# Performance work log

Hardware: AMD Instinct MI355X
Metric: run time of the kernel (lower is better)

## Reference

```python
import jax, jax.numpy as jnp
import numpy as np

S, B, D, H = 2048, 2, 1024, 16
DK = D // H


def rotate_half(x):
    # interleaved variant: pairs (x0,x1)->(-x1,x0)
    x1 = x[..., ::2]
    x2 = x[..., 1::2]
    return jnp.stack((-x2, x1), axis=-1).reshape(x.shape)


def apply_rope(x):
    # x: [B, H, S, dk]
    b, h, s, dk = x.shape
    pos = jnp.arange(s, dtype=jnp.float32)
    inv_freq = 1.0 / (10000.0 ** (jnp.arange(0, dk, 2, dtype=jnp.float32) / dk))
    freqs = jnp.einsum('i,j->ij', pos, inv_freq)          # [S, dk/2]
    emb = jnp.concatenate((freqs, freqs), axis=-1)        # [S, dk]  (non-interleaved cos/sin, as in source)
    cos = jnp.cos(emb)[None, None, :, :]
    sin = jnp.sin(emb)[None, None, :, :]
    return x * cos + rotate_half(x) * sin


def setup_inputs() -> dict:
    key = jax.random.key(0)
    ks = jax.random.split(key, 11)
    sc = 0.02
    return {
        'query': jax.random.normal(ks[0], (S, B, D), jnp.float32),
        'key':   jax.random.normal(ks[1], (S, B, D), jnp.float32),
        'value': jax.random.normal(ks[2], (S, B, D), jnp.float32),
        'wq': jax.random.normal(ks[3], (D, D), jnp.float32) * sc,
        'bq': jax.random.normal(ks[4], (D,), jnp.float32) * sc,
        'wk': jax.random.normal(ks[5], (D, D), jnp.float32) * sc,
        'bk': jax.random.normal(ks[6], (D,), jnp.float32) * sc,
        'wv': jax.random.normal(ks[7], (D, D), jnp.float32) * sc,
        'bv': jax.random.normal(ks[8], (D,), jnp.float32) * sc,
        'wo': jax.random.normal(ks[9], (D, D), jnp.float32) * sc,
        'bo': jax.random.normal(ks[10], (D,), jnp.float32) * sc,
    }


def reference(query, key, value, wq, bq, wk, bk, wv, bv, wo, bo):
    s_q, b, _ = query.shape
    s_k = key.shape[0]

    def split_heads(x, s):
        # [S,B,D] -> [B,H,S,dk]
        return x.transpose(1, 0, 2).reshape(b, s, H, DK).transpose(0, 2, 1, 3)

    Q = split_heads(query @ wq.T + bq, s_q)
    K = split_heads(key @ wk.T + bk, s_k)
    V = split_heads(value @ wv.T + bv, s_k)

    Q = apply_rope(Q)
    K = apply_rope(K)

    scores = jnp.einsum('bhqd,bhkd->bhqk', Q, K) / jnp.sqrt(jnp.float32(DK))
    attn = jax.nn.softmax(scores, axis=-1)
    out = jnp.einsum('bhqk,bhkd->bhqd', attn, V)          # [B,H,Sq,dk]
    out = out.transpose(0, 2, 1, 3).reshape(b, s_q, D)    # [B,Sq,D]
    out = out.transpose(1, 0, 2)                          # [Sq,B,D]
    return out @ wo.T + bo
```

## Files before the change

### kernel.cpp

```cpp
#include <hip/hip_runtime.h>
#include <cstdint>
#include <cstddef>

typedef __attribute__((ext_vector_type(4))) float f32x4;
typedef __attribute__((ext_vector_type(8))) float f32x8;
typedef __attribute__((ext_vector_type(16))) float f32x16;
typedef __attribute__((ext_vector_type(8))) __bf16 bf16x8;
typedef __attribute__((ext_vector_type(4))) __bf16 bf16x4;
typedef __attribute__((ext_vector_type(2))) __bf16 bf16x2;
typedef __attribute__((ext_vector_type(4))) unsigned int u32x4;
typedef unsigned short u16;

#define S_LEN 2048
#define BATCH 2
#define DMODEL 1024
#define NHEAD 16
#define HDK 64

__device__ __forceinline__ u16 f2bf(float f) {
    uint32_t u = __float_as_uint(f);
    u += 0x7FFFu + ((u >> 16) & 1u);
    return (u16)(u >> 16);
}

__device__ __forceinline__ void gload_lds16(const void* g, void* l) {
    __builtin_amdgcn_global_load_lds(
        (const __attribute__((address_space(1))) uint32_t*)g,
        (__attribute__((address_space(3))) uint32_t*)l, 16, 0, 0);
}

__device__ __forceinline__ unsigned pk2(float a, float b) {
    bf16x2 t;
    t[0] = (__bf16)a; t[1] = (__bf16)b;
    return __builtin_bit_cast(unsigned, t);
}

__device__ __forceinline__ f32x16 z16() {
    f32x16 v = {0.f,0.f,0.f,0.f,0.f,0.f,0.f,0.f,0.f,0.f,0.f,0.f,0.f,0.f,0.f,0.f};
    return v;
}

__global__ __launch_bounds__(256) void cvt_kernel(
    const float* __restrict__ a0, const float* __restrict__ a1, const float* __restrict__ a2,
    const float* __restrict__ a3, const float* __restrict__ a4, const float* __restrict__ a5,
    const float* __restrict__ a6,
    u16* __restrict__ o0, u16* __restrict__ o1, u16* __restrict__ o2,
    u16* __restrict__ o3, u16* __restrict__ o4, u16* __restrict__ o5,
    u16* __restrict__ o6)
{
    const int by = blockIdx.y;
    const float* s;
    u16* d;
    int n;
    switch (by) {
        case 0: s = a0; d = o0; n = 4194304; break;
        case 1: s = a1; d = o1; n = 4194304; break;
        case 2: s = a2; d = o2; n = 4194304; break;
        case 3: s = a3; d = o3; n = 1048576; break;
        case 4: s = a4; d = o4; n = 1048576; break;
        case 5: s = a5; d = o5; n = 1048576; break;
        default: s = a6; d = o6; n = 1048576; break;
    }
    int idx = (blockIdx.x * 256 + threadIdx.x) * 8;
    if (idx >= n) return;
    float4 f0 = *(const float4*)(s + idx);
    float4 f1 = *(const float4*)(s + idx + 4);
    alignas(16) u16 o[8] = {f2bf(f0.x), f2bf(f0.y), f2bf(f0.z), f2bf(f0.w),
                            f2bf(f1.x), f2bf(f1.y), f2bf(f1.z), f2bf(f1.w)};
    *(u32x4*)(d + idx) = *(const u32x4*)o;
}

__global__ __launch_bounds__(512) void qkv_kernel(
    const u16* __restrict__ X0, const u16* __restrict__ X1, const u16* __restrict__ X2,
    const u16* __restrict__ W0, const u16* __restrict__ W1, const u16* __restrict__ W2,
    const float* __restrict__ B0, const float* __restrict__ B1, const float* __restrict__ B2,
    u16* __restrict__ O0, u16* __restrict__ O1, u16* __restrict__ O2)
{
    __shared__ __align__(16) u16 lA[2][128 * 64];
    __shared__ __align__(16) u16 lB[2][128 * 64];
    const int tid = threadIdx.x, wid = tid >> 6, lane = tid & 63;
    const int l15 = lane & 15, l4 = lane >> 4;
    const int p = blockIdx.y * 32 + blockIdx.x;
    const int vid = (p & 7) * 96 + (p >> 3);
    const int bx = vid & 31, byv = vid >> 5;
    const int mat = byv >> 3;
    const u16* X = mat == 0 ? X0 : (mat == 1 ? X1 : X2);
    const u16* W = mat == 0 ? W0 : (mat == 1 ? W1 : W2);
    const float* bias = mat == 0 ? B0 : (mat == 1 ? B1 : B2);
    u16* O = mat == 0 ? O0 : (mat == 1 ? O1 : O2);
    const int m0 = bx * 128, n0 = (byv & 7) * 128;
    const int mw = (wid >> 1) * 32, nw = (wid & 1) * 64;

    f32x4 acc[2][4];
#pragma unroll
    for (int i = 0; i < 2; ++i)
#pragma unroll
        for (int j = 0; j < 4; ++j) acc[i][j] = (f32x4){0.f, 0.f, 0.f, 0.f};

#define QSTAGE(bufi, k0_) do {                                                \
        _Pragma("unroll")                                                     \
        for (int it = 0; it < 2; ++it) {                                      \
            int cc = it * 512 + tid;                                          \
            int row = cc >> 3, g = (cc & 7) ^ (row & 7);                      \
            gload_lds16(X + (size_t)(m0 + row) * 1024 + (k0_) + g * 8,        \
                        (char*)lA + (bufi) * 16384 + (cc & ~63) * 16);        \
            gload_lds16(W + (size_t)(n0 + row) * 1024 + (k0_) + g * 8,        \
                        (char*)lB + (bufi) * 16384 + (cc & ~63) * 16);        \
        }                                                                     \
    } while (0)

    QSTAGE(0, 0);
    for (int ks = 0; ks < 16; ++ks) {
        const int cur = ks & 1;
        if (ks < 15) {
            QSTAGE(cur ^ 1, (ks + 1) * 64);
            asm volatile("s_waitcnt vmcnt(4)" ::: "memory");
        } else {
            asm volatile("s_waitcnt vmcnt(0)" ::: "memory");
        }
        __builtin_amdgcn_s_barrier();
        const char* la = (const char*)lA + cur * 16384;
        const char* lb = (const char*)lB + cur * 16384;
        __builtin_amdgcn_s_setprio(1);
#pragma unroll
        for (int kk = 0; kk < 2; ++kk) {
            bf16x8 af[2], bfr[4];
#pragma unroll
            for (int f = 0; f < 2; ++f) {
                int ra = mw + f * 16 + l15;
                af[f] = *(const bf16x8*)(la + ra * 128 +
                        ((kk * 64 + l4 * 16) ^ ((ra & 7) << 4)));
            }
#pragma unroll
            for (int f = 0; f < 4; ++f) {
                int rb = nw + f * 16 + l15;
                bfr[f] = *(const bf16x8*)(lb + rb * 128 +
                        ((kk * 64 + l4 * 16) ^ ((rb & 7) << 4)));
            }
#pragma unroll
            for (int mf = 0; mf < 2; ++mf)
#pragma unroll
                for (int nf = 0; nf < 4; ++nf)
                    acc[mf][nf] = __builtin_amdgcn_mfma_f32_16x16x32_bf16(
                        af[mf], bfr[nf], acc[mf][nf], 0, 0, 0);
        }
        __builtin_amdgcn_s_setprio(0);
        __builtin_amdgcn_s_barrier();
    }
#undef QSTAGE

#pragma unroll
    for (int mf = 0; mf < 2; ++mf) {
#pragma unroll
        for (int nf = 0; nf < 4; ++nf) {
            int gcol = n0 + nw + nf * 16 + l15;
            float bval = bias[gcol];
            int h = gcol >> 6, d = gcol & 63;
            float invf = __expf(-(float)(d & 31) * 0.2878231366f);
#pragma unroll
            for (int i = 0; i < 4; ++i) {
                int grow = m0 + mw + mf * 16 + l4 * 4 + i;
                int s = grow >> 1, b = grow & 1;
                float v = acc[mf][nf][i] + bval;
                if (mat < 2) {
                    float p2 = __shfl_xor(v, 1);
                    float th = (float)s * invf;
                    float sn, cs;
                    __sincosf(th, &sn, &cs);
                    v = (d & 1) ? fmaf(p2, sn, v * cs) : fmaf(-p2, sn, v * cs);
                    if (mat == 0) v *= 0.18033688f;
                }
                O[((size_t)(b * NHEAD + h) * S_LEN + s) * HDK + d] = f2bf(v);
            }
        }
    }
}

__global__ __launch_bounds__(256) void vtrans_kernel(const u16* __restrict__ Vr, u16* __restrict__ Vt)
{
    __shared__ __align__(16) u16 t[64][72];
    const int tid = threadIdx.x, bh = blockIdx.y, s0 = blockIdx.x * 64;
    const u16* src = Vr + (size_t)bh * S_LEN * HDK;
    u16* dst = Vt + (size_t)bh * HDK * S_LEN;
    int r = tid >> 2, cbase = (tid & 3) * 16;
#pragma unroll
    for (int j = 0; j < 2; ++j)
        *(bf16x8*)&t[r][cbase + j * 8] =
            *(const bf16x8*)(const void*)(src + (size_t)(s0 + r) * HDK + cbase + j * 8);
    __syncthreads();
    int d = tid >> 2;
#pragma unroll
    for (int j = 0; j < 2; ++j) {
        alignas(16) u16 tmp[8];
#pragma unroll
        for (int x = 0; x < 8; ++x) {
            int lp = j * 8 + x;
            int sl = (lp & 3) | ((lp & 4) << 1) | ((lp & 8) >> 1);
            tmp[x] = t[cbase + sl][d];
        }
        *(bf16x8*)(void*)(dst + (size_t)d * S_LEN + s0 + cbase + j * 8) = *(const bf16x8*)tmp;
    }
}

__global__ __launch_bounds__(512, 4) void attn_kernel(
    const u16* __restrict__ Q, const u16* __restrict__ K,
    const u16* __restrict__ V, u16* __restrict__ O)
{
    __shared__ __align__(16) char smem[65536];
    const int tid = threadIdx.x, wid = tid >> 6, lane = tid & 63;
    const int g = wid >> 2, wv = wid & 3;
    const int l31 = lane & 31, hi = lane >> 5;
    const int p = blockIdx.y * 16 + blockIdx.x;
    const int vid = (p & 7) * 64 + (p >> 3);
    const int bh = vid >> 4, b = bh >> 4, h = bh & 15;
    const int q0 = (vid & 15) * 128;
    const u16* Qb = Q + (size_t)bh * S_LEN * HDK;
    const u16* Kb = K + (size_t)bh * S_LEN * HDK;
    const u16* Vb = V + (size_t)bh * HDK * S_LEN;

    const int qrow = q0 + wv * 32 + l31;
    bf16x8 aq[4];
#pragma unroll
    for (int ks = 0; ks < 4; ++ks)
        aq[ks] = *(const bf16x8*)(const void*)(Qb + (size_t)qrow * HDK + ks * 16 + hi * 8);

    f32x16 acc0 = z16(), acc1 = z16();
    float mrow = -1e30f, lpart = 0.f;

    char* gbase = smem + g * 32768;
    const int gt = tid & 255;
    const int srow = gt >> 3, lg = (gt & 7) ^ (srow & 7);
    char* sK = gbase + wv * 1024;
    char* sV = gbase + 8192 + wv * 1024;
    const u16* pk0 = Kb + (size_t)(g * 1024 + srow) * HDK + lg * 8;
    const u16* pk1 = pk0 + 32 * HDK;
    const u16* pv0 = Vb + (size_t)srow * S_LEN + g * 1024 + lg * 8;
    const u16* pv1 = pv0 + (size_t)32 * S_LEN;

    const int swl = (l31 & 7) << 4;
    const char* akr[4];
    const char* avr[4];
#pragma unroll
    for (int i = 0; i < 4; ++i) {
        akr[i] = gbase + l31 * 128 + ((i * 32 + hi * 16) ^ swl);
        avr[i] = gbase + 8192 + l31 * 128 + ((i * 32 + hi * 16) ^ swl);
    }

    gload_lds16(pk0, sK);
    gload_lds16(pk1, sK + 4096);
    gload_lds16(pv0, sV);
    gload_lds16(pv1, sV + 4096);
    pk0 += 4096; pk1 += 4096; pv0 += 64; pv1 += 64;

#define TILE(CUR_, STG_) do {                                                 \
    if (STG_) {                                                               \
        gload_lds16(pk0, sK + ((CUR_) ^ 1) * 16384);                          \
        gload_lds16(pk1, sK + ((CUR_) ^ 1) * 16384 + 4096);                   \
        gload_lds16(pv0, sV + ((CUR_) ^ 1) * 16384);                          \
        gload_lds16(pv1, sV + ((CUR_) ^ 1) * 16384 + 4096);                   \
        pk0 += 4096; pk1 += 4096; pv0 += 64; pv1 += 64;                       \
        asm volatile("s_waitcnt vmcnt(4)" ::: "memory");                      \
    } else {                                                                  \
        asm volatile("s_waitcnt vmcnt(0)" ::: "memory");                      \
    }                                                                         \
    __builtin_amdgcn_s_barrier();                                             \
    f32x16 s0 = z16(), s1 = z16();                                            \
    __builtin_amdgcn_s_setprio(1);                                            \
    _Pragma("unroll")                                                         \
    for (int ks = 0; ks < 4; ++ks) {                                          \
        bf16x8 a0 = *(const bf16x8*)(akr[ks] + (CUR_) * 16384);               \
        bf16x8 a1 = *(const bf16x8*)(akr[ks] + (CUR_) * 16384 + 4096);        \
        s0 = __builtin_amdgcn_mfma_f32_32x32x16_bf16(a0, aq[ks], s0, 0, 0, 0);\
        s1 = __builtin_amdgcn_mfma_f32_32x32x16_bf16(a1, aq[ks], s1, 0, 0, 0);\
    }                                                                         \
    __builtin_amdgcn_s_setprio(0);                                            \
    float c0 = fmaxf(fmaxf(s0[0], s0[1]), s0[2]);                             \
    c0 = fmaxf(fmaxf(c0, s0[3]), s0[4]);                                      \
    c0 = fmaxf(fmaxf(c0, s0[5]), s0[6]);                                      \
    c0 = fmaxf(c0, s0[7]);                                                    \
    float c1 = fmaxf(fmaxf(s0[8], s0[9]), s0[10]);                            \
    c1 = fmaxf(fmaxf(c1, s0[11]), s0[12]);                                    \
    c1 = fmaxf(fmaxf(c1, s0[13]), s0[14]);                                    \
    c1 = fmaxf(c1, s0[15]);                                                   \
    float c2 = fmaxf(fmaxf(s1[0], s1[1]), s1[2]);                             \
    c2 = fmaxf(fmaxf(c2, s1[3]), s1[4]);                                      \
    c2 = fmaxf(fmaxf(c2, s1[5]), s1[6]);                                      \
    c2 = fmaxf(c2, s1[7]);                                                    \
    float c3 = fmaxf(fmaxf(s1[8], s1[9]), s1[10]);                            \
    c3 = fmaxf(fmaxf(c3, s1[11]), s1[12]);                                    \
    c3 = fmaxf(fmaxf(c3, s1[13]), s1[14]);                                    \
    c3 = fmaxf(c3, s1[15]);                                                   \
    float pmax = fmaxf(fmaxf(c0, c1), fmaxf(c2, c3));                         \
    pmax = fmaxf(pmax, __shfl_xor(pmax, 32));                                 \
    if (!__all(pmax - mrow <= 11.5f)) {                                       \
        float mn = fmaxf(mrow, pmax);                                         \
        float sc = __builtin_amdgcn_exp2f(mrow - mn);                         \
        lpart *= sc;                                                          \
        acc0 *= sc; acc1 *= sc;                                               \
        mrow = mn;                                                            \
    }                                                                         \
    _Pragma("unroll")                                                         \
    for (int i = 0; i < 16; ++i) {                                            \
        s0[i] = __builtin_amdgcn_exp2f(s0[i] - mrow);                         \
        s1[i] = __builtin_amdgcn_exp2f(s1[i] - mrow);                         \
    }                                                                         \
    {                                                                         \
        f32x16 sm_ = s0 + s1;                                                 \
        f32x8 q8_ = __builtin_shufflevector(sm_, sm_, 0,1,2,3,4,5,6,7)        \
                  + __builtin_shufflevector(sm_, sm_, 8,9,10,11,12,13,14,15); \
        f32x4 q4_ = __builtin_shufflevector(q8_, q8_, 0,1,2,3)                \
                  + __builtin_shufflevector(q8_, q8_, 4,5,6,7);               \
        lpart += (q4_[0] + q4_[1]) + (q4_[2] + q4_[3]);                       \
    }                                                                         \
    __builtin_amdgcn_s_setprio(1);                                            \
    _Pragma("unroll")                                                         \
    for (int i = 0; i < 4; ++i) {                                             \
        const f32x16* cp = (i >> 1) ? &s1 : &s0;                              \
        const int e0 = (i & 1) * 8;                                           \
        u32x4 bw;                                                             \
        bw[0] = pk2((*cp)[e0 + 0], (*cp)[e0 + 1]);                            \
        bw[1] = pk2((*cp)[e0 + 2], (*cp)[e0 + 3]);                            \
        bw[2] = pk2((*cp)[e0 + 4], (*cp)[e0 + 5]);                            \
        bw[3] = pk2((*cp)[e0 + 6], (*cp)[e0 + 7]);                            \
        bf16x8 Bf = __builtin_bit_cast(bf16x8, bw);                           \
        bf16x8 av0 = *(const bf16x8*)(avr[i] + (CUR_) * 16384);               \
        bf16x8 av1 = *(const bf16x8*)(avr[i] + (CUR_) * 16384 + 4096);        \
        acc0 = __builtin_amdgcn_mfma_f32_32x32x16_bf16(av0, Bf, acc0, 0, 0, 0);\
        acc1 = __builtin_amdgcn_mfma_f32_32x32x16_bf16(av1, Bf, acc1, 0, 0, 0);\
    }                                                                         \
    __builtin_amdgcn_s_setprio(0);                                            \
    __builtin_amdgcn_s_barrier();                                             \
} while (0)

    for (int th = 0; th < 8; ++th) {
        TILE(0, 1);
        TILE(1, (th < 7));
    }
#undef TILE

    lpart += __shfl_xor(lpart, 32);
    float* exO = (float*)smem;
    float* exML = (float*)(smem + 36864);
    const int sl = wv * 64 + lane;
    if (g == 1) {
#pragma unroll
        for (int r4 = 0; r4 < 4; ++r4) {
            f32x4 w0 = {acc0[r4 * 4 + 0], acc0[r4 * 4 + 1], acc0[r4 * 4 + 2], acc0[r4 * 4 + 3]};
            f32x4 w1 = {acc1[r4 * 4 + 0], acc1[r4 * 4 + 1], acc1[r4 * 4 + 2], acc1[r4 * 4 + 3]};
            *(f32x4*)(exO + sl * 36 + r4 * 4) = w0;
            *(f32x4*)(exO + sl * 36 + 16 + r4 * 4) = w1;
        }
        exML[sl * 2] = mrow;
        exML[sl * 2 + 1] = lpart;
    }
    __syncthreads();
    if (g == 0) {
        float m1 = exML[sl * 2], l1 = exML[sl * 2 + 1];
        float mm = fmaxf(mrow, m1);
        float f0 = __builtin_amdgcn_exp2f(mrow - mm);
        float f1 = __builtin_amdgcn_exp2f(m1 - mm);
        float rl = 1.0f / (lpart * f0 + l1 * f1);
        f0 *= rl; f1 *= rl;
        u16* obase = O + ((size_t)qrow * BATCH + b) * DMODEL + h * HDK;
#pragma unroll
        for (int db = 0; db < 2; ++db) {
#pragma unroll
            for (int r4 = 0; r4 < 4; ++r4) {
                f32x4 part = *(const f32x4*)(exO + sl * 36 + db * 16 + r4 * 4);
                bf16x4 outv;
#pragma unroll
                for (int e = 0; e < 4; ++e) {
                    float own = db ? acc1[r4 * 4 + e] : acc0[r4 * 4 + e];
                    outv[e] = (__bf16)(own * f0 + part[e] * f1);
                }
                *(bf16x4*)(void*)(obase + db * 32 + 8 * r4 + 4 * hi) = outv;
            }
        }
    }
}

__global__ __launch_bounds__(256) void proj_kernel(
    const u16* __restrict__ A, const u16* __restrict__ W,
    const float* __restrict__ bias, float* __restrict__ out)
{
    __shared__ __align__(16) u16 lA[2][64 * 64];
    __shared__ __align__(16) u16 lB[2][128 * 64];
    const int tid = threadIdx.x, wid = tid >> 6, lane = tid & 63;
    const int l15 = lane & 15, l4 = lane >> 4;
    const int p = blockIdx.y * 8 + blockIdx.x;
    const int vid = (p & 7) * 64 + (p >> 3);
    const int m0 = (vid & 63) * 64, n0 = (vid >> 6) * 128;
    const int nw = wid * 32;

    f32x4 acc[4][2];
#pragma unroll
    for (int i = 0; i < 4; ++i)
#pragma unroll
        for (int j = 0; j < 2; ++j) acc[i][j] = (f32x4){0.f, 0.f, 0.f, 0.f};

#define PSTAGE(bufi, k0_) do {                                                \
        _Pragma("unroll")                                                     \
        for (int it = 0; it < 2; ++it) {                                      \
            int cc = it * 256 + tid;                                          \
            int row = cc >> 3, gg = (cc & 7) ^ (row & 7);                     \
            gload_lds16(A + (size_t)(m0 + row) * 1024 + (k0_) + gg * 8,       \
                        (char*)lA + (bufi) * 8192 + (cc & ~63) * 16);         \
        }                                                                     \
        _Pragma("unroll")                                                     \
        for (int it = 0; it < 4; ++it) {                                      \
            int cc = it * 256 + tid;                                          \
            int row = cc >> 3, gg = (cc & 7) ^ (row & 7);                     \
            gload_lds16(W + (size_t)(n0 + row) * 1024 + (k0_) + gg * 8,       \
                        (char*)lB + (bufi) * 16384 + (cc & ~63) * 16);        \
        }                                                                     \
    } while (0)

    PSTAGE(0, 0);
    for (int ks = 0; ks < 16; ++ks) {
        const int cur = ks & 1;
        if (ks < 15) {
            PSTAGE(cur ^ 1, (ks + 1) * 64);
            asm volatile("s_waitcnt vmcnt(6)" ::: "memory");
        } else {
            asm volatile("s_waitcnt vmcnt(0)" ::: "memory");
        }
        __builtin_amdgcn_s_barrier();
        const char* la = (const char*)lA + cur * 8192;
        const char* lb = (const char*)lB + cur * 16384;
        __builtin_amdgcn_s_setprio(1);
#pragma unroll
        for (int kk = 0; kk < 2; ++kk) {
            bf16x8 af[4], bfr[2];
#pragma unroll
            for (int f = 0; f < 4; ++f) {
                int ra = f * 16 + l15;
                af[f] = *(const bf16x8*)(la + ra * 128 +
                        ((kk * 64 + l4 * 16) ^ ((ra & 7) << 4)));
            }
#pragma unroll
            for (int f = 0; f < 2; ++f) {
                int rb = nw + f * 16 + l15;
                bfr[f] = *(const bf16x8*)(lb + rb * 128 +
                        ((kk * 64 + l4 * 16) ^ ((rb & 7) << 4)));
            }
#pragma unroll
            for (int mf = 0; mf < 4; ++mf)
#pragma unroll
                for (int nf = 0; nf < 2; ++nf)
                    acc[mf][nf] = __builtin_amdgcn_mfma_f32_16x16x32_bf16(
                        af[mf], bfr[nf], acc[mf][nf], 0, 0, 0);
        }
        __builtin_amdgcn_s_setprio(0);
        __builtin_amdgcn_s_barrier();
    }
#undef PSTAGE

#pragma unroll
    for (int mf = 0; mf < 4; ++mf) {
#pragma unroll
        for (int nf = 0; nf < 2; ++nf) {
            int gcol = n0 + nw + nf * 16 + l15;
            float bval = bias[gcol];
#pragma unroll
            for (int i = 0; i < 4; ++i) {
                int grow = m0 + mf * 16 + l4 * 4 + i;
                out[(size_t)grow * DMODEL + gcol] = acc[mf][nf][i] + bval;
            }
        }
    }
}

extern "C" void kernel_launch(void* const* d_in, const int* in_sizes, int n_in,
                              void* d_out, int out_size, void* d_ws, size_t ws_size,
                              hipStream_t stream)
{
    (void)in_sizes; (void)n_in; (void)out_size; (void)ws_size;
    const float* q  = (const float*)d_in[0];
    const float* k  = (const float*)d_in[1];
    const float* v  = (const float*)d_in[2];
    const float* wq = (const float*)d_in[3];
    const float* bq = (const float*)d_in[4];
    const float* wk = (const float*)d_in[5];
    const float* bk = (const float*)d_in[6];
    const float* wv = (const float*)d_in[7];
    const float* bv = (const float*)d_in[8];
    const float* wo = (const float*)d_in[9];
    const float* bo = (const float*)d_in[10];

    char* ws = (char*)d_ws;
    const size_t MB = 1024 * 1024;
    u16* XQ  = (u16*)(ws + 0 * MB);
    u16* XK  = (u16*)(ws + 8 * MB);
    u16* XV  = (u16*)(ws + 16 * MB);
    u16* WQb = (u16*)(ws + 24 * MB);
    u16* WKb = (u16*)(ws + 26 * MB);
    u16* WVb = (u16*)(ws + 28 * MB);
    u16* WOb = (u16*)(ws + 30 * MB);
    u16* QR  = (u16*)(ws + 32 * MB);
    u16* KR  = (u16*)(ws + 40 * MB);
    u16* VR  = (u16*)(ws + 48 * MB);
    u16* VT  = XK;
    u16* OA  = XQ;

    cvt_kernel<<<dim3(2048, 7), 256, 0, stream>>>(q, k, v, wq, wk, wv, wo,
                                                  XQ, XK, XV, WQb, WKb, WVb, WOb);
    qkv_kernel<<<dim3(32, 24), 512, 0, stream>>>(XQ, XK, XV, WQb, WKb, WVb,
                                                 bq, bk, bv, QR, KR, VR);
    vtrans_kernel<<<dim3(32, 32), 256, 0, stream>>>(VR, VT);
    attn_kernel<<<dim3(16, 32), 512, 0, stream>>>(QR, KR, VT, OA);
    proj_kernel<<<dim3(8, 64), 256, 0, stream>>>(OA, WOb, bo, (float*)d_out);
}
```

Baseline: 129.8 us.

## Halve QKV GEMM K-tile for more occupancy; tree-reduce softmax row max

The QKV projection GEMM now stages 32-wide K slices instead of 64-wide ones. This halves LDS per block (32KB to 16KB) and adds a min-blocks launch bound of 6 so more workgroups can be resident per CU, at the cost of twice as many loop iterations and barriers. The swizzle and wait counts are adjusted to the new tile. Separately, the attention score max is rewritten as a balanced tree of 3-input max ops to shorten the dependency chain and let the compiler use v_max3.

```diff
diff --git a/kernel.cpp b/kernel.cpp
--- a/kernel.cpp
+++ b/kernel.cpp
@@ -33,6 +33,10 @@
     bf16x2 t;
     t[0] = (__bf16)a; t[1] = (__bf16)b;
     return __builtin_bit_cast(unsigned, t);
+}
+
+__device__ __forceinline__ float fmax3(float a, float b, float c) {
+    return fmaxf(fmaxf(a, b), c);
 }
 
 __device__ __forceinline__ f32x16 z16() {
@@ -70,14 +74,14 @@
     *(u32x4*)(d + idx) = *(const u32x4*)o;
 }
 
-__global__ __launch_bounds__(512) void qkv_kernel(
+__global__ __launch_bounds__(512, 6) void qkv_kernel(
     const u16* __restrict__ X0, const u16* __restrict__ X1, const u16* __restrict__ X2,
     const u16* __restrict__ W0, const u16* __restrict__ W1, const u16* __restrict__ W2,
     const float* __restrict__ B0, const float* __restrict__ B1, const float* __restrict__ B2,
     u16* __restrict__ O0, u16* __restrict__ O1, u16* __restrict__ O2)
 {
-    __shared__ __align__(16) u16 lA[2][128 * 64];
-    __shared__ __align__(16) u16 lB[2][128 * 64];
+    __shared__ __align__(16) u16 lA[2][128 * 32];
+    __shared__ __align__(16) u16 lB[2][128 * 32];
     const int tid = threadIdx.x, wid = tid >> 6, lane = tid & 63;
     const int l15 = lane & 15, l4 = lane >> 4;
     const int p = blockIdx.y * 32 + blockIdx.x;
@@ -97,53 +101,47 @@
 #pragma unroll
         for (int j = 0; j < 4; ++j) acc[i][j] = (f32x4){0.f, 0.f, 0.f, 0.f};
 
+    const int srow = tid >> 2, sg = (tid & 3) ^ (srow & 3);
+
 #define QSTAGE(bufi, k0_) do {                                                \
-        _Pragma("unroll")                                                     \
-        for (int it = 0; it < 2; ++it) {                                      \
-            int cc = it * 512 + tid;                                          \
-            int row = cc >> 3, g = (cc & 7) ^ (row & 7);                      \
-            gload_lds16(X + (size_t)(m0 + row) * 1024 + (k0_) + g * 8,        \
-                        (char*)lA + (bufi) * 16384 + (cc & ~63) * 16);        \
-            gload_lds16(W + (size_t)(n0 + row) * 1024 + (k0_) + g * 8,        \
-                        (char*)lB + (bufi) * 16384 + (cc & ~63) * 16);        \
-        }                                                                     \
+        gload_lds16(X + (size_t)(m0 + srow) * 1024 + (k0_) + sg * 8,          \
+                    (char*)lA + (bufi) * 8192 + (tid & ~63) * 16);            \
+        gload_lds16(W + (size_t)(n0 + srow) * 1024 + (k0_) + sg * 8,          \
+                    (char*)lB + (bufi) * 8192 + (tid & ~63) * 16);            \
     } while (0)
 
     QSTAGE(0, 0);
-    for (int ks = 0; ks < 16; ++ks) {
+    for (int ks = 0; ks < 32; ++ks) {
         const int cur = ks & 1;
-        if (ks < 15) {
-            QSTAGE(cur ^ 1, (ks + 1) * 64);
-            asm volatile("s_waitcnt vmcnt(4)" ::: "memory");
+        if (ks < 31) {
+            QSTAGE(cur ^ 1, (ks + 1) * 32);
+            asm volatile("s_waitcnt vmcnt(2)" ::: "memory");
         } else {
             asm volatile("s_waitcnt vmcnt(0)" ::: "memory");
         }
         __builtin_amdgcn_s_barrier();
-        const char* la = (const char*)lA + cur * 16384;
-        const char* lb = (const char*)lB + cur * 16384;
+        const char* la = (const char*)lA + cur * 8192;
+        const char* lb = (const char*)lB + cur * 8192;
         __builtin_amdgcn_s_setprio(1);
-#pragma unroll
-        for (int kk = 0; kk < 2; ++kk) {
-            bf16x8 af[2], bfr[4];
-#pragma unroll
-            for (int f = 0; f < 2; ++f) {
-                int ra = mw + f * 16 + l15;
-                af[f] = *(const bf16x8*)(la + ra * 128 +
-                        ((kk * 64 + l4 * 16) ^ ((ra & 7) << 4)));
-            }
-#pragma unroll
-            for (int f = 0; f < 4; ++f) {
-                int rb = nw + f * 16 + l15;
-                bfr[f] = *(const bf16x8*)(lb + rb * 128 +
-                        ((kk * 64 + l4 * 16) ^ ((rb & 7) << 4)));
-            }
-#pragma unroll
-            for (int mf = 0; mf < 2; ++mf)
-#pragma unroll
-                for (int nf = 0; nf < 4; ++nf)
-                    acc[mf][nf] = __builtin_amdgcn_mfma_f32_16x16x32_bf16(
-                        af[mf], bfr[nf], acc[mf][nf], 0, 0, 0);
-        }
+        bf16x8 af[2], bfr[4];
+#pragma unroll
+        for (int f = 0; f < 2; ++f) {
+            int ra = mw + f * 16 + l15;
+            af[f] = *(const bf16x8*)(la + ra * 64 +
+                    ((l4 * 16) ^ ((ra & 3) << 4)));
+        }
+#pragma unroll
+        for (int f = 0; f < 4; ++f) {
+            int rb = nw + f * 16 + l15;
+            bfr[f] = *(const bf16x8*)(lb + rb * 64 +
+                    ((l4 * 16) ^ ((rb & 3) << 4)));
+        }
+#pragma unroll
+        for (int mf = 0; mf < 2; ++mf)
+#pragma unroll
+            for (int nf = 0; nf < 4; ++nf)
+                acc[mf][nf] = __builtin_amdgcn_mfma_f32_16x16x32_bf16(
+                    af[mf], bfr[nf], acc[mf][nf], 0, 0, 0);
         __builtin_amdgcn_s_setprio(0);
         __builtin_amdgcn_s_barrier();
     }
@@ -274,23 +272,21 @@
         s1 = __builtin_amdgcn_mfma_f32_32x32x16_bf16(a1, aq[ks], s1, 0, 0, 0);\
     }                                                                         \
     __builtin_amdgcn_s_setprio(0);                                            \
-    float c0 = fmaxf(fmaxf(s0[0], s0[1]), s0[2]);                             \
-    c0 = fmaxf(fmaxf(c0, s0[3]), s0[4]);                                      \
-    c0 = fmaxf(fmaxf(c0, s0[5]), s0[6]);                                      \
-    c0 = fmaxf(c0, s0[7]);                                                    \
-    float c1 = fmaxf(fmaxf(s0[8], s0[9]), s0[10]);                            \
-    c1 = fmaxf(fmaxf(c1, s0[11]), s0[12]);                                    \
-    c1 = fmaxf(fmaxf(c1, s0[13]), s0[14]);                                    \
-    c1 = fmaxf(c1, s0[15]);                                                   \
-    float c2 = fmaxf(fmaxf(s1[0], s1[1]), s1[2]);                             \
-    c2 = fmaxf(fmaxf(c2, s1[3]), s1[4]);                                      \
-    c2 = fmaxf(fmaxf(c2, s1[5]), s1[6]);                                      \
-    c2 = fmaxf(c2, s1[7]);                                                    \
-    float c3 = fmaxf(fmaxf(s1[8], s1[9]), s1[10]);                            \
-    c3 = fmaxf(fmaxf(c3, s1[11]), s1[12]);                                    \
-    c3 = fmaxf(fmaxf(c3, s1[13]), s1[14]);                                    \
-    c3 = fmaxf(c3, s1[15]);                                                   \
-    float pmax = fmaxf(fmaxf(c0, c1), fmaxf(c2, c3));                         \
+    float a0_ = fmax3(s0[0], s0[1], s0[2]);                                   \
+    float a1_ = fmax3(s0[3], s0[4], s0[5]);                                   \
+    float a2_ = fmax3(s0[6], s0[7], s0[8]);                                   \
+    float a3_ = fmax3(s0[9], s0[10], s0[11]);                                 \
+    float a4_ = fmax3(s0[12], s0[13], s0[14]);                                \
+    float b0_ = fmax3(s1[0], s1[1], s1[2]);                                   \
+    float b1_ = fmax3(s1[3], s1[4], s1[5]);                                   \
+    float b2_ = fmax3(s1[6], s1[7], s1[8]);                                   \
+    float b3_ = fmax3(s1[9], s1[10], s1[11]);                                 \
+    float b4_ = fmax3(s1[12], s1[13], s1[14]);                                \
+    float t0_ = fmax3(a0_, a1_, a2_);                                         \
+    float t1_ = fmax3(a3_, a4_, s0[15]);                                      \
+    float t2_ = fmax3(b0_, b1_, b2_);                                         \
+    float t3_ = fmax3(b3_, b4_, s1[15]);                                      \
+    float pmax = fmaxf(fmax3(t0_, t1_, t2_), t3_);                            \
     pmax = fmaxf(pmax, __shfl_xor(pmax, 32));                                 \
     if (!__all(pmax - mrow <= 11.5f)) {                                       \
         float mn = fmaxf(mrow, pmax);                                         \
```

Measured after the change: 125.1 us. 3.6% less time.
